# Kernel tuning notes

Hardware: AMD Instinct MI355X
Metric: run time of the kernel (lower is better)

The kernel has to match this reference:

```python
import jax, jax.numpy as jnp
import numpy as np

D_MODEL = 256
NHEAD = 8
HEAD_DIM = D_MODEL // NHEAD
LN_EPS = 1e-5


def _layernorm(x, g, b):
    mu = jnp.mean(x, axis=-1, keepdims=True)
    var = jnp.mean(jnp.square(x - mu), axis=-1, keepdims=True)
    return (x - mu) * jax.lax.rsqrt(var + LN_EPS) * g + b


def setup_inputs() -> dict:
    key = jax.random.key(0)
    ks = jax.random.split(key, 12)
    N, L, S, K = 2, 4800, 4800, 64
    x = jax.random.normal(ks[0], (N, L, D_MODEL), dtype=jnp.float32)
    source = jax.random.normal(ks[1], (N, S, D_MODEL), dtype=jnp.float32)
    # precomputed epipolar-band key indices per query ([N, L, K])
    epipolar_idx = jax.random.randint(ks[2], (N, L, K), 0, S, dtype=jnp.int32)
    w = lambda k, shape: (jax.random.normal(k, shape, dtype=jnp.float32) * 0.02)
    return {
        "x": x, "source": source, "epipolar_idx": epipolar_idx,
        "Wq": w(ks[3], (D_MODEL, D_MODEL)),
        "Wk": w(ks[4], (D_MODEL, D_MODEL)),
        "Wv": w(ks[5], (D_MODEL, D_MODEL)),
        "Wm": w(ks[6], (D_MODEL, D_MODEL)),
        "W1": w(ks[7], (2 * D_MODEL, 2 * D_MODEL)),
        "W2": w(ks[8], (2 * D_MODEL, D_MODEL)),
        "g1": jnp.ones((D_MODEL,), jnp.float32),
        "b1": jnp.zeros((D_MODEL,), jnp.float32),
        "g2": jnp.ones((D_MODEL,), jnp.float32),
        "b2": jnp.zeros((D_MODEL,), jnp.float32),
    }


def reference(x, source, epipolar_idx, Wq, Wk, Wv, Wm, W1, W2, g1, b1, g2, b2):
    N, L, _ = x.shape
    q = (x @ Wq).reshape(N, L, NHEAD, HEAD_DIM)            # [N,L,H,D]
    k = (source @ Wk).reshape(N, -1, NHEAD, HEAD_DIM)      # [N,S,H,D]
    v = (source @ Wv).reshape(N, -1, NHEAD, HEAD_DIM)
    # one-to-many gather: each query attends only to its epipolar-band keys
    gather = jax.vmap(lambda t, i: t[i])                   # [N,L,K,H,D]
    kg = gather(k, epipolar_idx)
    vg = gather(v, epipolar_idx)
    scale = 1.0 / jnp.sqrt(jnp.asarray(HEAD_DIM, x.dtype))
    scores = jnp.einsum('nlhd,nlkhd->nlhk', q, kg) * scale
    attn = jax.nn.softmax(scores, axis=-1)
    msg = jnp.einsum('nlhk,nlkhd->nlhd', attn, vg).reshape(N, L, D_MODEL)
    msg = _layernorm(msg @ Wm, g1, b1)
    h = jnp.concatenate([x, msg], axis=-1) @ W1            # [N,L,2C]
    h = jax.nn.relu(h) @ W2                                # [N,L,C]
    return x + _layernorm(h, g2, b2)
```

## Files before the change

kernel.cpp:

```cpp
#include <hip/hip_runtime.h>
#include <hip/hip_bf16.h>

#define D_MODEL 256
#define LQ 4800
#define NB 2
#define MROWS (NB * LQ)
#define LN_EPS 1e-5f

typedef unsigned int u32;
typedef unsigned short u16;
typedef unsigned char u8;
typedef __attribute__((ext_vector_type(8))) short bf16x8;
typedef __attribute__((ext_vector_type(4))) float f32x4;
typedef __attribute__((ext_vector_type(2))) float f32x2v;
typedef __attribute__((ext_vector_type(4))) u32 u32x4;
typedef __attribute__((ext_vector_type(2))) _Float16 f16x2;
typedef __attribute__((ext_vector_type(8))) _Float16 f16x8;

__device__ __forceinline__ u16 f2bf(float f) {
    __hip_bfloat16 h = __float2bfloat16(f);
    return *reinterpret_cast<u16*>(&h);
}
__device__ __forceinline__ float bf2f(u32 bits16) {
    return __uint_as_float(bits16 << 16);
}

__device__ __forceinline__ float dot2f16(u32 a, u32 b, float c) {
#if __has_builtin(__builtin_amdgcn_fdot2)
    return __builtin_amdgcn_fdot2(__builtin_bit_cast(f16x2, a),
                                  __builtin_bit_cast(f16x2, b), c, false);
#else
    f16x2 av = __builtin_bit_cast(f16x2, a), bv = __builtin_bit_cast(f16x2, b);
    c = fmaf((float)av.x, (float)bv.x, c);
    return fmaf((float)av.y, (float)bv.y, c);
#endif
}
__device__ __forceinline__ u32 pk_fma16(u32 a, u32 b, u32 c) {
    u32 d;
    asm("v_pk_fma_f16 %0, %1, %2, %3" : "=v"(d) : "v"(a), "v"(b), "v"(c));
    return d;
}
__device__ __forceinline__ u32 pk_add16(u32 a, u32 b) {
    u32 d;
    asm("v_pk_add_f16 %0, %1, %2" : "=v"(d) : "v"(a), "v"(b));
    return d;
}
__device__ __forceinline__ u32 pkrtz(float a, float b) {
    return __builtin_bit_cast(u32, __builtin_amdgcn_cvt_pkrtz(a, b));
}
__device__ __forceinline__ void gload_lds(const u16* src, u16* dst) {
    __builtin_amdgcn_global_load_lds(
        (const __attribute__((address_space(1))) u32*)src,
        (__attribute__((address_space(3))) u32*)dst, 16, 0, 0);
}
__device__ __forceinline__ void gload_lds_f32(const float* src, u32* dst) {
    __builtin_amdgcn_global_load_lds(
        (const __attribute__((address_space(1))) u32*)src,
        (__attribute__((address_space(3))) u32*)dst, 16, 0, 0);
}

__device__ __forceinline__ float fp8_to_f32_sw(u32 b) {
    u32 s = (b & 0x80) << 24;
    u32 e = (b >> 3) & 0xf;
    u32 m = b & 7;
    float mag = (e == 0) ? (float)m * 0.001953125f
                         : __uint_as_float(((e + 120) << 23) | (m << 20));
    return __uint_as_float(__float_as_uint(mag) | s);
}
__device__ __forceinline__ u32 f32_to_fp8_sw(float v) {
    u32 bits = __float_as_uint(v);
    u32 s = (bits >> 24) & 0x80;
    float a = fabsf(v);
    if (!(a >= 0.0009765625f)) return s;
    if (a >= 448.f) return s | 0x7e;
    if (a < 0.015625f) {
        u32 m = (u32)(a * 512.f + 0.5f);
        if (m > 7) m = 7;
        return s | m;
    }
    int e = ((bits >> 23) & 0xff) - 127;
    u32 mant = bits & 0x7fffff;
    u32 m3 = mant >> 20, rem = mant & 0xfffff;
    if (rem > 0x80000 || (rem == 0x80000 && (m3 & 1))) { m3++; if (m3 == 8) { m3 = 0; e++; } }
    if (e > 8) return s | 0x7e;
    return s | ((u32)(e + 7) << 3) | m3;
}
__device__ __forceinline__ void fp8x4_to_2xf16(u32 v, u32& lo, u32& hi) {
#if __has_builtin(__builtin_amdgcn_cvt_pk_f32_fp8)
    f32x2v a = __builtin_amdgcn_cvt_pk_f32_fp8((int)v, false);
    f32x2v b = __builtin_amdgcn_cvt_pk_f32_fp8((int)v, true);
    lo = pkrtz(a[0], a[1]);
    hi = pkrtz(b[0], b[1]);
#else
    lo = pkrtz(fp8_to_f32_sw(v & 0xff), fp8_to_f32_sw((v >> 8) & 0xff));
    hi = pkrtz(fp8_to_f32_sw((v >> 16) & 0xff), fp8_to_f32_sw(v >> 24));
#endif
}
__device__ __forceinline__ u8 f32_to_fp8b(float v) {
#if __has_builtin(__builtin_amdgcn_cvt_pk_fp8_f32)
    return (u8)(__builtin_amdgcn_cvt_pk_fp8_f32(v, v, 0, false) & 0xff);
#else
    return (u8)f32_to_fp8_sw(v);
#endif
}

__global__ __launch_bounds__(256) void prep_kernel(
    const float* __restrict__ Wq, const float* __restrict__ Wk,
    const float* __restrict__ Wv, const float* __restrict__ Wm,
    const float* __restrict__ W1, const float* __restrict__ W2,
    u16* __restrict__ Wqkvh, u16* __restrict__ Wmt,
    u16* __restrict__ W1bt, u16* __restrict__ W2t)
{
    __shared__ float tile[16][17];
    const int t = threadIdx.x, tx = t & 15, ty = t >> 4;
    int sub = blockIdx.x;

    const float* W; int Nd, tn, tk, drow, dcol, ldt; u16* dst; bool f16o = false;
    if (sub < 768) {
        W = sub < 256 ? Wq : (sub < 512 ? Wk : Wv);
        int s = sub & 255; Nd = 256; tn = s % 16; tk = s / 16;
        dst = Wqkvh; drow = (sub >> 8) * 256 + tn * 16; dcol = tk * 16; ldt = 256; f16o = true;
    } else if (sub < 1024) {
        W = Wm; int s = sub - 768; Nd = 256; tn = s % 16; tk = s / 16;
        dst = Wmt; drow = tn * 16; dcol = tk * 16; ldt = 256;
    } else if (sub < 2048) {
        W = W1; int s = sub - 1024; Nd = 512; tn = s % 32; tk = s / 32;
        if (tk < 16) { dst = Wqkvh; drow = 768 + tn * 16; dcol = tk * 16; ldt = 256; f16o = true; }
        else         { dst = W1bt;  drow = tn * 16; dcol = (tk - 16) * 16; ldt = 256; }
    } else {
        W = W2; int s = sub - 2048; Nd = 256; tn = s % 16; tk = s / 16;
        dst = W2t; drow = tn * 16; dcol = tk * 16; ldt = 512;
    }
    tile[ty][tx] = W[(size_t)(tk * 16 + ty) * Nd + tn * 16 + tx];
    __syncthreads();
    float v = tile[tx][ty];
    u16 o;
    if (f16o) { _Float16 h = (_Float16)v; o = __builtin_bit_cast(u16, h); }
    else      o = f2bf(v);
    dst[(size_t)(drow + ty) * ldt + dcol + tx] = o;
}

__global__ __launch_bounds__(256) void qkvh_kernel(
    const float* __restrict__ x, const float* __restrict__ source,
    const u16* __restrict__ Wqkvh,
    u16* __restrict__ qb, u8* __restrict__ kb8, u8* __restrict__ vb8,
    u16* __restrict__ hx)
{
    __shared__ __align__(16) float As32[64 * 32];
    __shared__ __align__(16) u16 Bs[128 * 32];

    const int t = threadIdx.x, l = t & 63, w = t >> 6;
    const int m0 = blockIdx.y * 64, n0 = blockIdx.x * 128;
    const int wr = w >> 1, wc = w & 1;
    const float* Ap = (n0 < 256 || n0 >= 768) ? x : source;

    const int srow = l >> 2, sch = (l & 3) ^ (srow & 3);
    const int arow8 = l >> 3, acw = (l & 7) ^ (arow8 & 7);
    const int r = l & 15, ch = l >> 4;

    f32x4 acc[2][4];
#pragma unroll
    for (int i = 0; i < 2; ++i)
#pragma unroll
        for (int j = 0; j < 4; ++j) acc[i][j] = (f32x4){0.f, 0.f, 0.f, 0.f};

    for (int k0 = 0; k0 < 256; k0 += 32) {
#pragma unroll
        for (int h = 0; h < 2; ++h) {
            const float* asrc = Ap + (size_t)(m0 + w * 16 + h * 8 + arow8) * 256 + k0 + acw * 4;
            gload_lds_f32(asrc, (u32*)As32 + w * 512 + h * 256);
        }
#pragma unroll
        for (int g = 0; g < 2; ++g) {
            int grp = w * 2 + g;
            gload_lds(Wqkvh + (size_t)(n0 + grp * 16 + srow) * 256 + k0 + sch * 8,
                      Bs + grp * 512);
        }
        __syncthreads();

        f16x8 af[2];
#pragma unroll
        for (int i = 0; i < 2; ++i) {
            int ar = wr * 32 + i * 16 + r;
            int s0 = (2 * ch) ^ (ar & 7), s1 = (2 * ch + 1) ^ (ar & 7);
            f32x4 alo = *(const f32x4*)((const char*)As32 + ar * 128 + s0 * 16);
            f32x4 ahi = *(const f32x4*)((const char*)As32 + ar * 128 + s1 * 16);
            u32x4 pk = { pkrtz(alo.x, alo.y), pkrtz(alo.z, alo.w),
                         pkrtz(ahi.x, ahi.y), pkrtz(ahi.z, ahi.w) };
            af[i] = __builtin_bit_cast(f16x8, pk);
        }
#pragma unroll
        for (int j = 0; j < 4; ++j) {
            int br = wc * 64 + j * 16 + r;
            f16x8 bf = *(const f16x8*)((const char*)Bs + br * 64 + ((ch ^ (r & 3)) * 16));
#pragma unroll
            for (int i = 0; i < 2; ++i)
                acc[i][j] = __builtin_amdgcn_mfma_f32_16x16x32_f16(af[i], bf, acc[i][j], 0, 0, 0);
        }
        __syncthreads();
    }

    const int q4 = l >> 4;
#pragma unroll
    for (int i = 0; i < 2; ++i)
#pragma unroll
        for (int j = 0; j < 4; ++j) {
            int col = n0 + wc * 64 + j * 16 + r;
#pragma unroll
            for (int reg = 0; reg < 4; ++reg) {
                int row = m0 + wr * 32 + i * 16 + q4 * 4 + reg;
                float vv = acc[i][j][reg];
                if (col < 256) {
                    _Float16 hv = (_Float16)vv;
                    qb[(size_t)row * 256 + col] = __builtin_bit_cast(u16, hv);
                } else if (col < 512) {
                    kb8[(size_t)row * 256 + (col - 256)] = f32_to_fp8b(vv);
                } else if (col < 768) {
                    vb8[(size_t)row * 256 + (col - 512)] = f32_to_fp8b(vv);
                } else {
                    hx[(size_t)row * 512 + (col - 768)] = f2bf(vv);
                }
            }
        }
}

__global__ __launch_bounds__(256) void wm_w1_kernel(
    const u16* __restrict__ msg, const u16* __restrict__ Wmt,
    const u16* __restrict__ W1bt, const u16* __restrict__ hx,
    const float* __restrict__ g1, const float* __restrict__ b1,
    u16* __restrict__ h1b)
{
    __shared__ __align__(16) u16 As[32 * 32];
    __shared__ __align__(16) u16 Bs[512 * 32];
    __shared__ __align__(16) u16 mln[32 * 256];
    __shared__ float2 red[32][2];

    const int t = threadIdx.x, l = t & 63, w = t >> 6;
    const int m0 = blockIdx.x * 32;
    const int srow = l >> 2, sch = (l & 3) ^ (srow & 3);
    const int r = l & 15, ch = l >> 4, q4 = l >> 4;

    {
        const int wr = w >> 1, wc = w & 1;
        f32x4 acc[8];
#pragma unroll
        for (int j = 0; j < 8; ++j) acc[j] = (f32x4){0.f, 0.f, 0.f, 0.f};

        for (int k0 = 0; k0 < 256; k0 += 32) {
            if (w < 2)
                gload_lds(msg + (size_t)(m0 + w * 16 + srow) * 256 + k0 + sch * 8, As + w * 512);
#pragma unroll
            for (int g = 0; g < 4; ++g) {
                int grp = w * 4 + g;
                gload_lds(Wmt + (size_t)(grp * 16 + srow) * 256 + k0 + sch * 8, Bs + grp * 512);
            }
            __syncthreads();
            bf16x8 af = *(const bf16x8*)((const char*)As + (wr * 16 + r) * 64 + ((ch ^ (r & 3)) * 16));
#pragma unroll
            for (int j = 0; j < 8; ++j) {
                int br = wc * 128 + j * 16 + r;
                bf16x8 bf = *(const bf16x8*)((const char*)Bs + br * 64 + ((ch ^ (r & 3)) * 16));
                acc[j] = __builtin_amdgcn_mfma_f32_16x16x32_bf16(af, bf, acc[j], 0, 0, 0);
            }
            __syncthreads();
        }

        float rs[4], rq[4];
#pragma unroll
        for (int reg = 0; reg < 4; ++reg) {
            float s = 0.f, sq = 0.f;
#pragma unroll
            for (int j = 0; j < 8; ++j) { float vv = acc[j][reg]; s += vv; sq += vv * vv; }
            rs[reg] = s; rq[reg] = sq;
        }
#pragma unroll
        for (int off = 1; off <= 8; off <<= 1)
#pragma unroll
            for (int reg = 0; reg < 4; ++reg) {
                rs[reg] += __shfl_xor(rs[reg], off);
                rq[reg] += __shfl_xor(rq[reg], off);
            }
        if (r == 0)
#pragma unroll
            for (int reg = 0; reg < 4; ++reg)
                red[wr * 16 + q4 * 4 + reg][wc] = make_float2(rs[reg], rq[reg]);
        __syncthreads();

#pragma unroll
        for (int reg = 0; reg < 4; ++reg) {
            int row = wr * 16 + q4 * 4 + reg;
            float sum = red[row][0].x + red[row][1].x;
            float sq  = red[row][0].y + red[row][1].y;
            float mu  = sum * 0.00390625f;
            float var = sq * 0.00390625f - mu * mu;
            float rstd = rsqrtf(var + LN_EPS);
#pragma unroll
            for (int j = 0; j < 8; ++j) {
                int col = wc * 128 + j * 16 + r;
                float vv = (acc[j][reg] - mu) * rstd * g1[col] + b1[col];
                int cc = col >> 3, slot = cc ^ (row & 7);
                *(u16*)((char*)mln + row * 512 + slot * 16 + (col & 7) * 2) = f2bf(vv);
            }
        }
        __syncthreads();
    }

    {
        f32x4 acc2[2][8];
#pragma unroll
        for (int i = 0; i < 2; ++i)
#pragma unroll
            for (int j = 0; j < 8; ++j) acc2[i][j] = (f32x4){0.f, 0.f, 0.f, 0.f};

        for (int k0 = 0; k0 < 256; k0 += 32) {
#pragma unroll
            for (int g = 0; g < 8; ++g) {
                int row = w * 128 + g * 16 + srow;
                gload_lds(W1bt + (size_t)row * 256 + k0 + sch * 8, Bs + (w * 8 + g) * 512);
            }
            __syncthreads();
            bf16x8 af2[2];
#pragma unroll
            for (int i = 0; i < 2; ++i) {
                int ar = i * 16 + r;
                int c0 = (k0 >> 3) + ch;
                af2[i] = *(const bf16x8*)((const char*)mln + ar * 512 + ((c0 ^ (ar & 7)) * 16));
            }
#pragma unroll
            for (int j = 0; j < 8; ++j) {
                int br = w * 128 + j * 16 + r;
                bf16x8 bf = *(const bf16x8*)((const char*)Bs + br * 64 + ((ch ^ (r & 3)) * 16));
#pragma unroll
                for (int i = 0; i < 2; ++i)
                    acc2[i][j] = __builtin_amdgcn_mfma_f32_16x16x32_bf16(af2[i], bf, acc2[i][j], 0, 0, 0);
            }
            __syncthreads();
        }

#pragma unroll
        for (int i = 0; i < 2; ++i)
#pragma unroll
            for (int j = 0; j < 8; ++j) {
                int col = w * 128 + j * 16 + r;
#pragma unroll
                for (int reg = 0; reg < 4; ++reg) {
                    int row = i * 16 + q4 * 4 + reg;
                    size_t oidx = (size_t)(m0 + row) * 512 + col;
                    float vv = acc2[i][j][reg] + bf2f((u32)hx[oidx]);
                    vv = fmaxf(vv, 0.f);
                    h1b[oidx] = f2bf(vv);
                }
            }
    }
}

template<bool RESID, bool OUT_BF16>
__global__ __launch_bounds__(256) void gemm_ln_kernel(
    const u16* __restrict__ A, int lda,
    const u16* __restrict__ Bt, int ldb,
    const float* __restrict__ g, const float* __restrict__ b,
    const float* __restrict__ xres,
    void* __restrict__ Cout, int K)
{
    __shared__ __align__(16) u16 As[32 * 32];
    __shared__ __align__(16) u16 Bs[256 * 32];
    __shared__ float2 red[32][2];

    const int t  = threadIdx.x, l = t & 63, w = t >> 6;
    const int m0 = blockIdx.x * 32;
    const int wr = w >> 1, wc = w & 1;
    const int srow = l >> 2, sch = (l & 3) ^ (srow & 3);
    const int r = l & 15, ch = l >> 4, q4 = l >> 4;

    f32x4 acc[8];
#pragma unroll
    for (int j = 0; j < 8; ++j) acc[j] = (f32x4){0.f, 0.f, 0.f, 0.f};

    for (int k0 = 0; k0 < K; k0 += 32) {
        if (w < 2)
            gload_lds(A + (size_t)(m0 + w * 16 + srow) * lda + k0 + sch * 8, As + w * 512);
#pragma unroll
        for (int gg = 0; gg < 4; ++gg) {
            int grp = w * 4 + gg;
            gload_lds(Bt + (size_t)(grp * 16 + srow) * ldb + k0 + sch * 8, Bs + grp * 512);
        }
        __syncthreads();
        bf16x8 af = *(const bf16x8*)((const char*)As + (wr * 16 + r) * 64 + ((ch ^ (r & 3)) * 16));
#pragma unroll
        for (int j = 0; j < 8; ++j) {
            int br = wc * 128 + j * 16 + r;
            bf16x8 bf = *(const bf16x8*)((const char*)Bs + br * 64 + ((ch ^ (r & 3)) * 16));
            acc[j] = __builtin_amdgcn_mfma_f32_16x16x32_bf16(af, bf, acc[j], 0, 0, 0);
        }
        __syncthreads();
    }

    float rs[4], rq[4];
#pragma unroll
    for (int reg = 0; reg < 4; ++reg) {
        float s = 0.f, sq = 0.f;
#pragma unroll
        for (int j = 0; j < 8; ++j) { float vv = acc[j][reg]; s += vv; sq += vv * vv; }
        rs[reg] = s; rq[reg] = sq;
    }
#pragma unroll
    for (int off = 1; off <= 8; off <<= 1)
#pragma unroll
        for (int reg = 0; reg < 4; ++reg) {
            rs[reg] += __shfl_xor(rs[reg], off);
            rq[reg] += __shfl_xor(rq[reg], off);
        }
    if (r == 0)
#pragma unroll
        for (int reg = 0; reg < 4; ++reg)
            red[wr * 16 + q4 * 4 + reg][wc] = make_float2(rs[reg], rq[reg]);
    __syncthreads();

    float gj[8], bj[8];
#pragma unroll
    for (int j = 0; j < 8; ++j) {
        int col = wc * 128 + j * 16 + r;
        gj[j] = g[col]; bj[j] = b[col];
    }

#pragma unroll
    for (int reg = 0; reg < 4; ++reg) {
        int row = wr * 16 + q4 * 4 + reg;
        float sum = red[row][0].x + red[row][1].x;
        float sq  = red[row][0].y + red[row][1].y;
        float mu  = sum * 0.00390625f;
        float var = sq * 0.00390625f - mu * mu;
        float rstd = rsqrtf(var + LN_EPS);
#pragma unroll
        for (int j = 0; j < 8; ++j) {
            int col = wc * 128 + j * 16 + r;
            float vv = (acc[j][reg] - mu) * rstd * gj[j] + bj[j];
            size_t oidx = (size_t)(m0 + row) * 256 + col;
            if (RESID) vv += xres[oidx];
            if (OUT_BF16) ((u16*)Cout)[oidx] = f2bf(vv);
            else          ((float*)Cout)[oidx] = vv;
        }
    }
}

__global__ __launch_bounds__(256, 8) void attn_kernel(
    const u16* __restrict__ q, const u8* __restrict__ k8,
    const u8* __restrict__ v8, const int* __restrict__ idx,
    u16* __restrict__ msg)
{
    const int t  = threadIdx.x;
    const int l  = t & 63;
    const int hp = t >> 6;
    const int bid = blockIdx.x;
    const int x8 = bid & 7, jj = bid >> 3;
    const int qi = (x8 < 4) ? (x8 * 1200 + jj) : (LQ + (x8 - 4) * 1200 + jj);
    const int n  = qi / LQ;
    const size_t srcbase8 = (size_t)n * LQ * 256;

    const int o = l >> 3;
    const int c = l & 7;

    const int* idxp = idx + (size_t)qi * 64;
    int rows[8];
#pragma unroll
    for (int i = 0; i < 8; ++i) rows[i] = idxp[i * 8 + o];

    const size_t hoff8 = (size_t)hp * 64 + c * 8;
    const size_t hoffq = (size_t)hp * 64 + c * 8;

    uint2 kd[8];
#pragma unroll
    for (int i = 0; i < 8; ++i)
        kd[i] = *(const uint2*)(k8 + srcbase8 + (size_t)rows[i] * 256 + hoff8);
    uint4 qc = *(const uint4*)(q + (size_t)qi * 256 + hoffq);

    float s[8];
#pragma unroll
    for (int i = 0; i < 8; ++i) {
        u32 k0l, k0h, k1l, k1h;
        fp8x4_to_2xf16(kd[i].x, k0l, k0h);
        fp8x4_to_2xf16(kd[i].y, k1l, k1h);
        float si = 0.f;
        si = dot2f16(k0l, qc.x, si);
        si = dot2f16(k0h, qc.y, si);
        si = dot2f16(k1l, qc.z, si);
        si = dot2f16(k1h, qc.w, si);
        si += __shfl_xor(si, 1);
        si += __shfl_xor(si, 2);
        s[i] = si * 0.17677669529663687f;
    }

    uint2 vd[8];
#pragma unroll
    for (int i = 0; i < 8; ++i)
        vd[i] = *(const uint2*)(v8 + srcbase8 + (size_t)rows[i] * 256 + hoff8);

    float mx = s[0];
#pragma unroll
    for (int i = 1; i < 8; ++i) mx = fmaxf(mx, s[i]);
    mx = fmaxf(mx, __shfl_xor(mx, 8));
    mx = fmaxf(mx, __shfl_xor(mx, 16));
    mx = fmaxf(mx, __shfl_xor(mx, 32));
    float p[8], sum = 0.f;
#pragma unroll
    for (int i = 0; i < 8; ++i) { p[i] = __expf(s[i] - mx); sum += p[i]; }
    sum += __shfl_xor(sum, 8);
    sum += __shfl_xor(sum, 16);
    sum += __shfl_xor(sum, 32);
    float inv = 1.f / sum;

    u32 A0 = 0, A1 = 0, A2 = 0, A3 = 0;
#pragma unroll
    for (int i = 0; i < 8; ++i) {
        float pi = p[i] * inv;
        u32 pp = pkrtz(pi, pi);
        u32 v0l, v0h, v1l, v1h;
        fp8x4_to_2xf16(vd[i].x, v0l, v0h);
        fp8x4_to_2xf16(vd[i].y, v1l, v1h);
        A0 = pk_fma16(pp, v0l, A0);
        A1 = pk_fma16(pp, v0h, A1);
        A2 = pk_fma16(pp, v1l, A2);
        A3 = pk_fma16(pp, v1h, A3);
    }

    const bool ob0 = (o & 1) != 0;
    const bool ob1 = (o & 2) != 0;
    {
        u32 t0 = ob0 ? A0 : A2;
        u32 t1 = ob0 ? A1 : A3;
        t0 = __shfl_xor((int)t0, 8);
        t1 = __shfl_xor((int)t1, 8);
        A0 = pk_add16(ob0 ? A2 : A0, t0);
        A1 = pk_add16(ob0 ? A3 : A1, t1);
    }
    {
        u32 u0 = ob1 ? A0 : A1;
        u0 = __shfl_xor((int)u0, 16);
        A0 = pk_add16(ob1 ? A1 : A0, u0);
    }
    A0 = pk_add16(A0, (u32)__shfl_xor((int)A0, 32));

    if (o < 4) {
        int j = 2 * (o & 1) + ((o >> 1) & 1);
        f16x2 hv = __builtin_bit_cast(f16x2, A0);
        u32 packed = (u32)f2bf((float)hv.x) | ((u32)f2bf((float)hv.y) << 16);
        *(u32*)(msg + (size_t)qi * 256 + hp * 64 + c * 8 + j * 2) = packed;
    }
}

extern "C" void kernel_launch(void* const* d_in, const int* in_sizes, int n_in,
                              void* d_out, int out_size, void* d_ws, size_t ws_size,
                              hipStream_t stream)
{
    const float* x      = (const float*)d_in[0];
    const float* source = (const float*)d_in[1];
    const int*   eidx   = (const int*)d_in[2];
    const float* Wq     = (const float*)d_in[3];
    const float* Wk     = (const float*)d_in[4];
    const float* Wv     = (const float*)d_in[5];
    const float* Wm     = (const float*)d_in[6];
    const float* W1     = (const float*)d_in[7];
    const float* W2     = (const float*)d_in[8];
    const float* g1     = (const float*)d_in[9];
    const float* b1     = (const float*)d_in[10];
    const float* g2     = (const float*)d_in[11];
    const float* b2     = (const float*)d_in[12];
    float* out = (float*)d_out;

    char* ws = (char*)d_ws;
    const size_t SZB = (size_t)MROWS * 256 * 2;
    u16* qb     = (u16*)(ws);
    u8*  kb8    = (u8*)(ws + SZB);
    u8*  vb8    = (u8*)(ws + SZB + SZB / 2);
    u16* msgb   = (u16*)(ws + 2 * SZB);
    u16* hx     = (u16*)(ws + 3 * SZB);
    u16* h1b    = (u16*)(ws + 5 * SZB);
    u16* Wqkvh  = (u16*)(ws + 7 * SZB);
    u16* Wmt    = Wqkvh + 1280 * 256;
    u16* W1bt   = Wmt + 256 * 256;
    u16* W2t    = W1bt + 512 * 256;

    dim3 blk(256);

    prep_kernel<<<dim3(2560), blk, 0, stream>>>(Wq, Wk, Wv, Wm, W1, W2,
                                                Wqkvh, Wmt, W1bt, W2t);

    qkvh_kernel<<<dim3(10, 150), blk, 0, stream>>>(x, source, Wqkvh, qb, kb8, vb8, hx);

    attn_kernel<<<dim3(MROWS), blk, 0, stream>>>(qb, kb8, vb8, eidx, msgb);

    wm_w1_kernel<<<dim3(300), blk, 0, stream>>>(msgb, Wmt, W1bt, hx, g1, b1, h1b);

    gemm_ln_kernel<true, false><<<dim3(300), blk, 0, stream>>>(
        h1b, 512, W2t, 512, g2, b2, x, out, 512);
}
```

Baseline: 93.95 us.

## Pre-convert x/source to fp16 and widen QKVH GEMM tile to 256 columns

The prep kernel now also converts x and source from fp32 to fp16 in a separate pass. The QKVH GEMM therefore loads fp16 A tiles directly, with no in-loop fp32-to-fp16 packing. Its N tile doubles to 256, so each block computes a 64x256 output with twice the accumulators. This cuts the A re-reads across column blocks and halves the grid. In exchange it adds an extra global write and read of the converted activations, raises register pressure, and leaves fewer blocks.

```diff
diff --git a/kernel.cpp b/kernel.cpp
--- a/kernel.cpp
+++ b/kernel.cpp
@@ -24,6 +24,10 @@
 __device__ __forceinline__ float bf2f(u32 bits16) {
     return __uint_as_float(bits16 << 16);
 }
+__device__ __forceinline__ u16 f2h(float f) {
+    _Float16 h = (_Float16)f;
+    return __builtin_bit_cast(u16, h);
+}
 
 __device__ __forceinline__ float dot2f16(u32 a, u32 b, float c) {
 #if __has_builtin(__builtin_amdgcn_fdot2)
@@ -49,11 +53,6 @@
     return __builtin_bit_cast(u32, __builtin_amdgcn_cvt_pkrtz(a, b));
 }
 __device__ __forceinline__ void gload_lds(const u16* src, u16* dst) {
-    __builtin_amdgcn_global_load_lds(
-        (const __attribute__((address_space(1))) u32*)src,
-        (__attribute__((address_space(3))) u32*)dst, 16, 0, 0);
-}
-__device__ __forceinline__ void gload_lds_f32(const float* src, u32* dst) {
     __builtin_amdgcn_global_load_lds(
         (const __attribute__((address_space(1))) u32*)src,
         (__attribute__((address_space(3))) u32*)dst, 16, 0, 0);
@@ -105,16 +104,30 @@
 }
 
 __global__ __launch_bounds__(256) void prep_kernel(
+    const float* __restrict__ x, const float* __restrict__ source,
     const float* __restrict__ Wq, const float* __restrict__ Wk,
     const float* __restrict__ Wv, const float* __restrict__ Wm,
     const float* __restrict__ W1, const float* __restrict__ W2,
+    u16* __restrict__ xh, u16* __restrict__ sh,
     u16* __restrict__ Wqkvh, u16* __restrict__ Wmt,
     u16* __restrict__ W1bt, u16* __restrict__ W2t)
 {
     __shared__ float tile[16][17];
     const int t = threadIdx.x, tx = t & 15, ty = t >> 4;
-    int sub = blockIdx.x;
-
+    int bid = blockIdx.x;
+
+    if (bid < 4800) {
+        const float* src = bid < 2400 ? x : source;
+        u16* dst = bid < 2400 ? xh : sh;
+        int b = bid < 2400 ? bid : bid - 2400;
+        int i = (b * 256 + t) * 4;
+        float4 v = *reinterpret_cast<const float4*>(src + i);
+        ushort4 o;
+        o.x = f2h(v.x); o.y = f2h(v.y); o.z = f2h(v.z); o.w = f2h(v.w);
+        *reinterpret_cast<ushort4*>(dst + i) = o;
+        return;
+    }
+    int sub = bid - 4800;
     const float* W; int Nd, tn, tk, drow, dcol, ldt; u16* dst; bool f16o = false;
     if (sub < 768) {
         W = sub < 256 ? Wq : (sub < 512 ? Wk : Wv);
@@ -134,45 +147,37 @@
     tile[ty][tx] = W[(size_t)(tk * 16 + ty) * Nd + tn * 16 + tx];
     __syncthreads();
     float v = tile[tx][ty];
-    u16 o;
-    if (f16o) { _Float16 h = (_Float16)v; o = __builtin_bit_cast(u16, h); }
-    else      o = f2bf(v);
-    dst[(size_t)(drow + ty) * ldt + dcol + tx] = o;
+    dst[(size_t)(drow + ty) * ldt + dcol + tx] = f16o ? f2h(v) : f2bf(v);
 }
 
 __global__ __launch_bounds__(256) void qkvh_kernel(
-    const float* __restrict__ x, const float* __restrict__ source,
+    const u16* __restrict__ xh, const u16* __restrict__ sh,
     const u16* __restrict__ Wqkvh,
     u16* __restrict__ qb, u8* __restrict__ kb8, u8* __restrict__ vb8,
     u16* __restrict__ hx)
 {
-    __shared__ __align__(16) float As32[64 * 32];
-    __shared__ __align__(16) u16 Bs[128 * 32];
+    __shared__ __align__(16) u16 As[64 * 32];
+    __shared__ __align__(16) u16 Bs[256 * 32];
 
     const int t = threadIdx.x, l = t & 63, w = t >> 6;
-    const int m0 = blockIdx.y * 64, n0 = blockIdx.x * 128;
+    const int m0 = blockIdx.y * 64, n0 = blockIdx.x * 256;
     const int wr = w >> 1, wc = w & 1;
-    const float* Ap = (n0 < 256 || n0 >= 768) ? x : source;
+    const u16* Ap = (n0 == 256 || n0 == 512) ? sh : xh;
 
     const int srow = l >> 2, sch = (l & 3) ^ (srow & 3);
-    const int arow8 = l >> 3, acw = (l & 7) ^ (arow8 & 7);
     const int r = l & 15, ch = l >> 4;
 
-    f32x4 acc[2][4];
+    f32x4 acc[2][8];
 #pragma unroll
     for (int i = 0; i < 2; ++i)
 #pragma unroll
-        for (int j = 0; j < 4; ++j) acc[i][j] = (f32x4){0.f, 0.f, 0.f, 0.f};
+        for (int j = 0; j < 8; ++j) acc[i][j] = (f32x4){0.f, 0.f, 0.f, 0.f};
 
     for (int k0 = 0; k0 < 256; k0 += 32) {
-#pragma unroll
-        for (int h = 0; h < 2; ++h) {
-            const float* asrc = Ap + (size_t)(m0 + w * 16 + h * 8 + arow8) * 256 + k0 + acw * 4;
-            gload_lds_f32(asrc, (u32*)As32 + w * 512 + h * 256);
-        }
-#pragma unroll
-        for (int g = 0; g < 2; ++g) {
-            int grp = w * 2 + g;
+        gload_lds(Ap + (size_t)(m0 + w * 16 + srow) * 256 + k0 + sch * 8, As + w * 512);
+#pragma unroll
+        for (int g = 0; g < 4; ++g) {
+            int grp = w * 4 + g;
             gload_lds(Wqkvh + (size_t)(n0 + grp * 16 + srow) * 256 + k0 + sch * 8,
                       Bs + grp * 512);
         }
@@ -182,16 +187,11 @@
 #pragma unroll
         for (int i = 0; i < 2; ++i) {
             int ar = wr * 32 + i * 16 + r;
-            int s0 = (2 * ch) ^ (ar & 7), s1 = (2 * ch + 1) ^ (ar & 7);
-            f32x4 alo = *(const f32x4*)((const char*)As32 + ar * 128 + s0 * 16);
-            f32x4 ahi = *(const f32x4*)((const char*)As32 + ar * 128 + s1 * 16);
-            u32x4 pk = { pkrtz(alo.x, alo.y), pkrtz(alo.z, alo.w),
-                         pkrtz(ahi.x, ahi.y), pkrtz(ahi.z, ahi.w) };
-            af[i] = __builtin_bit_cast(f16x8, pk);
-        }
-#pragma unroll
-        for (int j = 0; j < 4; ++j) {
-            int br = wc * 64 + j * 16 + r;
+            af[i] = *(const f16x8*)((const char*)As + ar * 64 + ((ch ^ (r & 3)) * 16));
+        }
+#pragma unroll
+        for (int j = 0; j < 8; ++j) {
+            int br = wc * 128 + j * 16 + r;
             f16x8 bf = *(const f16x8*)((const char*)Bs + br * 64 + ((ch ^ (r & 3)) * 16));
 #pragma unroll
             for (int i = 0; i < 2; ++i)
@@ -204,15 +204,14 @@
 #pragma unroll
     for (int i = 0; i < 2; ++i)
 #pragma unroll
-        for (int j = 0; j < 4; ++j) {
-            int col = n0 + wc * 64 + j * 16 + r;
+        for (int j = 0; j < 8; ++j) {
+            int col = n0 + wc * 128 + j * 16 + r;
 #pragma unroll
             for (int reg = 0; reg < 4; ++reg) {
                 int row = m0 + wr * 32 + i * 16 + q4 * 4 + reg;
                 float vv = acc[i][j][reg];
                 if (col < 256) {
-                    _Float16 hv = (_Float16)vv;
-                    qb[(size_t)row * 256 + col] = __builtin_bit_cast(u16, hv);
+                    qb[(size_t)row * 256 + col] = f2h(vv);
                 } else if (col < 512) {
                     kb8[(size_t)row * 256 + (col - 256)] = f32_to_fp8b(vv);
                 } else if (col < 768) {
@@ -575,17 +574,19 @@
     u16* msgb   = (u16*)(ws + 2 * SZB);
     u16* hx     = (u16*)(ws + 3 * SZB);
     u16* h1b    = (u16*)(ws + 5 * SZB);
-    u16* Wqkvh  = (u16*)(ws + 7 * SZB);
+    u16* xh     = (u16*)(ws + 7 * SZB);
+    u16* sh     = (u16*)(ws + 8 * SZB);
+    u16* Wqkvh  = (u16*)(ws + 9 * SZB);
     u16* Wmt    = Wqkvh + 1280 * 256;
     u16* W1bt   = Wmt + 256 * 256;
     u16* W2t    = W1bt + 512 * 256;
 
     dim3 blk(256);
 
-    prep_kernel<<<dim3(2560), blk, 0, stream>>>(Wq, Wk, Wv, Wm, W1, W2,
-                                                Wqkvh, Wmt, W1bt, W2t);
-
-    qkvh_kernel<<<dim3(10, 150), blk, 0, stream>>>(x, source, Wqkvh, qb, kb8, vb8, hx);
+    prep_kernel<<<dim3(7360), blk, 0, stream>>>(x, source, Wq, Wk, Wv, Wm, W1, W2,
+                                                xh, sh, Wqkvh, Wmt, W1bt, W2t);
+
+    qkvh_kernel<<<dim3(5, 150), blk, 0, stream>>>(xh, sh, Wqkvh, qb, kb8, vb8, hx);
 
     attn_kernel<<<dim3(MROWS), blk, 0, stream>>>(qb, kb8, vb8, eidx, msgb);
 
```

Measured after the change: 92.77 us, median of 2. No clear change (-1.3%).
